# Kernel tuning notes

Measured on AMD Instinct MI355X. Metric: run time of the kernel, lower is better.

## Reference

```python
import jax, jax.numpy as jnp
import numpy as np

SEQ_LEN = 256
VOCAB = 50000
EMBED = 300
PROJ = 200
ATT = 200
CLS = 3
B = 128


def setup_inputs() -> dict:
    key = jax.random.key(0)
    ks = jax.random.split(key, 16)
    s = lambda d: 1.0 / np.sqrt(d)
    return {
        "x1": jax.random.randint(ks[0], (B, SEQ_LEN), 0, VOCAB, dtype=jnp.int32),
        "x2": jax.random.randint(ks[1], (B, SEQ_LEN), 0, VOCAB, dtype=jnp.int32),
        "emb": jax.random.normal(ks[2], (VOCAB, EMBED), jnp.float32),
        # intra-attention forward_product FC (shared for x1/x2 via AUTO_REUSE)
        "Wi": jax.random.normal(ks[3], (EMBED, ATT), jnp.float32) * s(EMBED),
        "bi": jnp.zeros((ATT,), jnp.float32),
        "b_dist": jax.random.normal(ks[4], (1,), jnp.float32) * 0.1,
        # embed-scope projection (input is concat[x, xp] -> 2*EMBED), linear
        "Wp": jax.random.normal(ks[5], (2 * EMBED, PROJ), jnp.float32) * s(2 * EMBED),
        "bp": jnp.zeros((PROJ,), jnp.float32),
        # attent forward_product FC (shared)
        "Wa": jax.random.normal(ks[6], (PROJ, ATT), jnp.float32) * s(PROJ),
        "ba": jnp.zeros((ATT,), jnp.float32),
        # compare FC (shared, dim = input dim = 2*PROJ)
        "Wc": jax.random.normal(ks[7], (2 * PROJ, 2 * PROJ), jnp.float32) * s(2 * PROJ),
        "bc": jnp.zeros((2 * PROJ,), jnp.float32),
        # aggregate FC -> class logits (linear)
        "Wg": jax.random.normal(ks[8], (4 * PROJ, CLS), jnp.float32) * s(4 * PROJ),
        "bg": jnp.zeros((CLS,), jnp.float32),
    }


def _seq_mask(x):
    # tf.count_nonzero + tf.sequence_mask -> [B, L, 1] float mask
    size = jnp.sum((x != 0).astype(jnp.float32), axis=1)  # [B]
    m = (jnp.arange(SEQ_LEN)[None, :] < size[:, None]).astype(jnp.float32)
    return m[:, :, None]


def _intra(x, Wi, bi, b_dist):
    # forward_product on (x, x): relu FC then bilinear product -> [B, L, L]
    f = jax.nn.relu(x @ Wi + bi)
    att = jnp.einsum("bid,bjd->bij", f, f)
    idx = jnp.arange(SEQ_LEN)
    dist = jnp.abs(idx[None, :] - idx[:, None])
    bias = b_dist[0] * (dist >= 10).astype(jnp.float32)  # [L, L]
    xp = jnp.einsum("bik,bkj->bij", jax.nn.softmax(att + bias[None], axis=2), x)
    return jnp.concatenate([x, xp], axis=2)  # [B, L, 2*EMBED]


def reference(x1, x2, emb, Wi, bi, b_dist, Wp, bp, Wa, ba, Wc, bc, Wg, bg):
    mask1, mask2 = _seq_mask(x1), _seq_mask(x2)  # [B, L, 1]

    # embedding lookup with L2-normalized table
    emb_n = emb / jnp.linalg.norm(emb, axis=1, keepdims=True)
    e1, e2 = emb_n[x1], emb_n[x2]  # [B, L, EMBED]

    # intra-attention (distance-biased self alignment), doubles feature dim
    h1 = _intra(e1, Wi, bi, b_dist)
    h2 = _intra(e2, Wi, bi, b_dist)

    # linear projection to PROJ
    p1 = h1 @ Wp + bp  # [B, L, PROJ]
    p2 = h2 @ Wp + bp

    # attent: forward_product sim + mask + dual-axis softmax alignments
    a1 = jax.nn.relu(p1 @ Wa + ba)
    a2 = jax.nn.relu(p2 @ Wa + ba)
    sim = jnp.einsum("bid,bjd->bij", a1, a2)  # [B, L, L]
    sim = sim * (mask1 * jnp.swapaxes(mask2, 1, 2))
    alpha = jnp.einsum("bki,bkj->bij", jax.nn.softmax(sim, axis=1), p1)
    beta = jnp.einsum("bik,bkj->bij", jax.nn.softmax(sim, axis=2), p2)

    # compare (shared relu FC)
    v1 = jax.nn.relu(jnp.concatenate([p1, beta], 2) @ Wc + bc)
    v2 = jax.nn.relu(jnp.concatenate([p2, alpha], 2) @ Wc + bc)

    # aggregate: masked sum pooling + linear classifier
    v1 = jnp.sum(v1 * mask1, axis=1)  # [B, 2*PROJ]
    v2 = jnp.sum(v2 * mask2, axis=1)
    return jnp.concatenate([v1, v2], 1) @ Wg + bg  # [B, CLS]
```

## Files before the change

### kernel.cpp

```cpp
#include <hip/hip_runtime.h>
#include <math.h>

#define LSEQ 256
#define NB   128

typedef unsigned short u16;
typedef unsigned int   u32;
typedef __attribute__((ext_vector_type(8))) short bf16x8;
typedef __attribute__((ext_vector_type(4))) float f32x4;

static __device__ __forceinline__ u16 f2bf(float x) {
    union { float f; u32 u; } v; v.f = x;
    const u32 r = v.u + 0x7fffu + ((v.u >> 16) & 1u);
    return (u16)(r >> 16);
}
static __device__ __forceinline__ u32 cvt_pk(float lo, float hi) {
    u32 r; asm("v_cvt_pk_bf16_f32 %0, %1, %2" : "=v"(r) : "v"(lo), "v"(hi));
    return r;
}
static __device__ __forceinline__ u16 f2bf_fast(float x) {
    u32 r; asm("v_cvt_pk_bf16_f32 %0, %1, %1" : "=v"(r) : "v"(x));
    return (u16)r;
}
static __device__ __forceinline__ void glds16(const u16* src, u16* dst) {
    __builtin_amdgcn_global_load_lds(
        (const __attribute__((address_space(1))) u32*)src,
        (__attribute__((address_space(3))) u32*)dst, 16, 0, 0);
}
static __device__ __forceinline__ void bar_lgkm() {
    asm volatile("s_waitcnt lgkmcnt(0)" ::: "memory");
    __builtin_amdgcn_s_barrier();
}
static __device__ __forceinline__ void bar_vm0() {
    asm volatile("s_waitcnt vmcnt(0)" ::: "memory");
    __builtin_amdgcn_s_barrier();
}

template<int EPI, bool BIAS, bool RELU>
__global__ __launch_bounds__(512)
void gemm(const u16* __restrict__ A, int lda,
          const u16* __restrict__ B, int ldb,
          u16* __restrict__ C, int ldc,
          const float* __restrict__ bias, int Nbias,
          float* __restrict__ pool, const float* __restrict__ pmask,
          int K, int Nwrite)
{
    __shared__ u16 As[128 * 64];
    __shared__ u16 Bs[256 * 64];

    const int m0 = blockIdx.y * 128;
    const int n0 = blockIdx.x * 256;
    const int t = threadIdx.x;
    const int lane = t & 63;
    const int w = t >> 6;
    const int wm = w >> 2;
    const int wn = w & 3;
    const int lr = lane & 15;
    const int lg = lane >> 4;

    f32x4 acc[4][4] = {};

    for (int k0 = 0; k0 < K; k0 += 64) {
#pragma unroll
        for (int i = 0; i < 2; ++i) {
            const int ch = w * 2 + i;
            const int row = (ch << 3) + (lane >> 3);
            const int slot = (lane & 7) ^ (row & 7);
            glds16(A + (long long)(m0 + row) * lda + k0 + (slot << 3), &As[ch << 9]);
        }
#pragma unroll
        for (int i = 0; i < 4; ++i) {
            const int ch = w * 4 + i;
            const int row = (ch << 3) + (lane >> 3);
            const int slot = (lane & 7) ^ (row & 7);
            glds16(B + (long long)(n0 + row) * ldb + k0 + (slot << 3), &Bs[ch << 9]);
        }
        __syncthreads();
#pragma unroll
        for (int kk = 0; kk < 2; ++kk) {
            bf16x8 af[4], bf[4];
#pragma unroll
            for (int mi = 0; mi < 4; ++mi) {
                const int row = wm * 64 + mi * 16 + lr;
                const int slot = ((kk << 2) + lg) ^ (row & 7);
                af[mi] = *reinterpret_cast<const bf16x8*>(&As[row * 64 + (slot << 3)]);
            }
#pragma unroll
            for (int ni = 0; ni < 4; ++ni) {
                const int row = wn * 64 + ni * 16 + lr;
                const int slot = ((kk << 2) + lg) ^ (row & 7);
                bf[ni] = *reinterpret_cast<const bf16x8*>(&Bs[row * 64 + (slot << 3)]);
            }
#pragma unroll
            for (int mi = 0; mi < 4; ++mi)
#pragma unroll
                for (int ni = 0; ni < 4; ++ni)
                    acc[mi][ni] = __builtin_amdgcn_mfma_f32_16x16x32_bf16(
                        af[mi], bf[ni], acc[mi][ni], 0, 0, 0);
        }
        __syncthreads();
    }

    const int rbase = lg << 2;
    if (EPI == 0) {
#pragma unroll
        for (int ni = 0; ni < 4; ++ni) {
            const int gc = n0 + wn * 64 + ni * 16 + lr;
            if (gc >= Nwrite) continue;
            float bcv = 0.f;
            if (BIAS) bcv = (gc < Nbias) ? bias[gc] : 0.f;
#pragma unroll
            for (int mi = 0; mi < 4; ++mi) {
#pragma unroll
                for (int r = 0; r < 4; ++r) {
                    const long long gr = m0 + wm * 64 + mi * 16 + rbase + r;
                    float x = acc[mi][ni][r];
                    if (BIAS) x += bcv;
                    if (RELU) x = fmaxf(x, 0.f);
                    C[gr * ldc + gc] = f2bf_fast(x);
                }
            }
        }
    } else {
        __syncthreads();
        float* pool_s = reinterpret_cast<float*>(As);
        for (int i = t; i < 256; i += 512) pool_s[i] = 0.f;
        __syncthreads();
        const int b_lin = m0 >> 8;
        const int side  = b_lin >> 7;
        const int bb    = b_lin & 127;
        const float* mk = pmask + b_lin * 256 + (m0 & 255);
        float mrow[4][4];
#pragma unroll
        for (int mi = 0; mi < 4; ++mi)
#pragma unroll
            for (int r = 0; r < 4; ++r)
                mrow[mi][r] = mk[wm * 64 + mi * 16 + rbase + r];
#pragma unroll
        for (int ni = 0; ni < 4; ++ni) {
            const int lc = wn * 64 + ni * 16 + lr;
            const int gc = n0 + lc;
            const float bcv = (BIAS && gc < Nbias) ? bias[gc] : 0.f;
            float cs = 0.f;
#pragma unroll
            for (int mi = 0; mi < 4; ++mi)
#pragma unroll
                for (int r = 0; r < 4; ++r)
                    cs += fmaxf(acc[mi][ni][r] + bcv, 0.f) * mrow[mi][r];
            cs += __shfl_xor(cs, 16, 64);
            cs += __shfl_xor(cs, 32, 64);
            if (lg == 0) atomicAdd(&pool_s[lc], cs);
        }
        __syncthreads();
        for (int i = t; i < 256; i += 512) {
            const int gc = n0 + i;
            if (gc < Nwrite) atomicAdd(&pool[bb * 800 + side * 400 + gc], pool_s[i]);
        }
    }
}

template<int MODE>
__global__ __launch_bounds__(512)
void fattn(const u16* __restrict__ QK, u16* __restrict__ Hb,
           u16* __restrict__ CMP, u16* __restrict__ CMP2,
           const float* __restrict__ M1, const float* __restrict__ M2,
           const float* __restrict__ b_dist)
{
    constexpr int NVT = (MODE == 0) ? 5 : 4;
    __shared__ __align__(16) char shmem[MODE == 0 ? 57344 : 49152];
    u16* Ks0 = (u16*)shmem;
    u16* Ks1 = (u16*)(shmem + 16384);
    u16* Qs0 = (u16*)(shmem + 32768);
    u16* Qs1 = (u16*)(shmem + 40960);
    u16* Pc = (u16*)shmem;
    u16* Vc = (u16*)(shmem + 16384);
    float* red  = (float*)shmem;
    float* red2 = red + 512;

    const int bz = blockIdx.x;
    int b, half, rowoff, ldv, ldc, Nwrite;
    const u16 *Kp, *Qp, *Vp;
    u16* Cp;
    const float *mrow = nullptr, *mcol = nullptr;
    if (MODE == 0) {
        b = (bz & 7) + (bz >> 4) * 8;
        half = (bz >> 3) & 1;
        Kp = QK + (long long)b * 65536;
        Qp = Kp;
        Vp = Hb + (long long)b * 163840; ldv = 640;
        Cp = Hb + (long long)b * 163840 + half * 128 * 640 + 320;
        ldc = 640; Nwrite = 320; rowoff = half * 128;
    } else {
        const int xcd = bz & 7, j = bz >> 3;
        const int sib = j & 3;
        b = xcd + (j >> 2) * 8;
        half = sib & 1;
        const int v = sib >> 1;
        const u16* a1 = QK + (long long)b * 65536;
        const u16* a2 = QK + 32768LL * 256 + (long long)b * 65536;
        u16* P1 = CMP  + (long long)b * 114688;
        u16* P2 = CMP2 + (long long)b * 114688;
        if (v == 0) { Qp = a1 + half * 128 * 256; Kp = a2; Vp = P2;
                      Cp = P1 + half * 128 * 448 + 200;
                      mrow = M1 + b * 256 + half * 128; mcol = M2 + b * 256; }
        else        { Qp = a2 + half * 128 * 256; Kp = a1; Vp = P1;
                      Cp = P2 + half * 128 * 448 + 200;
                      mrow = M2 + b * 256 + half * 128; mcol = M1 + b * 256; }
        ldv = 448; ldc = 448; Nwrite = 248; rowoff = 0;
    }

    const int t = threadIdx.x, lane = t & 63, w = t >> 6;
    const int lr = lane & 15, lg = lane >> 4;
    const int wk = w >> 1, wr = w & 1;
    const int wr2 = w >> 2, wc = w & 3;

    f32x4 acc[4][4] = {};
    {
        const int krow = (lane >> 2);
        const int kslot = (lane & 3) ^ (krow & 3);
#pragma unroll
        for (int i = 0; i < 2; ++i) {
            const int ch = w * 2 + i;
            glds16(Kp + (long long)(ch * 16 + krow) * 256 + (kslot << 3), Ks0 + (ch << 9));
        }
        if (MODE != 0)
            glds16(Qp + (long long)(w * 16 + krow) * 256 + (kslot << 3), Qs0 + (w << 9));
        for (int it = 0; it < 8; ++it) {
            bar_vm0();
            if (it < 7) {
                const int k0 = (it + 1) * 32;
                u16* kb2 = ((it + 1) & 1) ? Ks1 : Ks0;
#pragma unroll
                for (int i = 0; i < 2; ++i) {
                    const int ch = w * 2 + i;
                    glds16(Kp + (long long)(ch * 16 + krow) * 256 + k0 + (kslot << 3),
                           kb2 + (ch << 9));
                }
                if (MODE != 0) {
                    u16* qb2 = ((it + 1) & 1) ? Qs1 : Qs0;
                    glds16(Qp + (long long)(w * 16 + krow) * 256 + k0 + (kslot << 3),
                           qb2 + (w << 9));
                }
            }
            const u16* kb = (it & 1) ? Ks1 : Ks0;
            const u16* qb = (MODE == 0) ? kb : ((it & 1) ? Qs1 : Qs0);
            bf16x8 kf[4], qf[4];
#pragma unroll
            for (int ki = 0; ki < 4; ++ki) {
                const int row = wk * 64 + ki * 16 + lr;
                kf[ki] = *reinterpret_cast<const bf16x8*>(
                    &kb[row * 32 + ((lg ^ (row & 3)) << 3)]);
            }
#pragma unroll
            for (int qi = 0; qi < 4; ++qi) {
                const int row = (MODE == 0 ? rowoff : 0) + wr * 64 + qi * 16 + lr;
                qf[qi] = *reinterpret_cast<const bf16x8*>(
                    &qb[row * 32 + ((lg ^ (row & 3)) << 3)]);
            }
            __builtin_amdgcn_s_setprio(1);
#pragma unroll
            for (int ki = 0; ki < 4; ++ki)
#pragma unroll
                for (int qi = 0; qi < 4; ++qi)
                    acc[ki][qi] = __builtin_amdgcn_mfma_f32_16x16x32_bf16(
                        kf[ki], qf[qi], acc[ki][qi], 0, 0, 0);
            __builtin_amdgcn_s_setprio(0);
        }
    }

    if (MODE == 1) {
        float mr[4], mc[4][4];
#pragma unroll
        for (int qi = 0; qi < 4; ++qi) mr[qi] = mrow[wr * 64 + qi * 16 + lr];
#pragma unroll
        for (int ki = 0; ki < 4; ++ki)
#pragma unroll
            for (int r = 0; r < 4; ++r)
                mc[ki][r] = mcol[wk * 64 + ki * 16 + (lg << 2) + r];
#pragma unroll
        for (int ki = 0; ki < 4; ++ki)
#pragma unroll
            for (int qi = 0; qi < 4; ++qi)
#pragma unroll
                for (int r = 0; r < 4; ++r)
                    acc[ki][qi][r] *= mr[qi] * mc[ki][r];
    } else {
        const float bd = b_dist[0];
#pragma unroll
        for (int ki = 0; ki < 4; ++ki) {
            const int kb_ = wk * 64 + ki * 16;
#pragma unroll
            for (int qi = 0; qi < 4; ++qi) {
                const int qb_ = rowoff + wr * 64 + qi * 16;
                const int diff = qb_ - kb_;
                if (diff >= -24 && diff <= 24) {
                    const int irow = qb_ + lr;
                    const int jc0  = kb_ + (lg << 2);
#pragma unroll
                    for (int r = 0; r < 4; ++r) {
                        const int d = irow - (jc0 + r);
                        const int ad = d < 0 ? -d : d;
                        if (ad < 10) acc[ki][qi][r] -= bd;
                    }
                }
            }
        }
    }

    const int n4  = (t & 63) << 2;
    const int k8v = (t >> 6) << 3;
    const int n4b = 256 + ((t & 15) << 2);
    const int k8b = (t >> 4) << 3;
    uint2 vreg[8], vtail[8];
#pragma unroll
    for (int i = 0; i < 8; ++i)
        vreg[i] = *reinterpret_cast<const uint2*>(Vp + (long long)(k8v + i) * ldv + n4);
    if (NVT == 5) {
        if (t < 128) {
#pragma unroll
            for (int i = 0; i < 8; ++i)
                vtail[i] = *reinterpret_cast<const uint2*>(Vp + (long long)(k8b + i) * ldv + n4b);
        }
    }

    float mx[4];
#pragma unroll
    for (int qi = 0; qi < 4; ++qi) {
        float m_ = -1e30f;
#pragma unroll
        for (int ki = 0; ki < 4; ++ki)
#pragma unroll
            for (int r = 0; r < 4; ++r) m_ = fmaxf(m_, acc[ki][qi][r]);
        m_ = fmaxf(m_, __shfl_xor(m_, 16, 64));
        m_ = fmaxf(m_, __shfl_xor(m_, 32, 64));
        mx[qi] = m_;
    }
    if (lg == 0) {
#pragma unroll
        for (int qi = 0; qi < 4; ++qi)
            red[(wr * 64 + qi * 16 + lr) * 4 + wk] = mx[qi];
    }
    bar_lgkm();
    float sm[4];
#pragma unroll
    for (int qi = 0; qi < 4; ++qi) {
        const int row = wr * 64 + qi * 16 + lr;
        const float m_ = fmaxf(fmaxf(red[row * 4 + 0], red[row * 4 + 1]),
                               fmaxf(red[row * 4 + 2], red[row * 4 + 3]));
        float s_ = 0.f;
#pragma unroll
        for (int ki = 0; ki < 4; ++ki)
#pragma unroll
            for (int r = 0; r < 4; ++r) {
                const float e_ = __expf(acc[ki][qi][r] - m_);
                acc[ki][qi][r] = e_;
                s_ += e_;
            }
        s_ += __shfl_xor(s_, 16, 64);
        s_ += __shfl_xor(s_, 32, 64);
        sm[qi] = s_;
    }
    if (lg == 0) {
#pragma unroll
        for (int qi = 0; qi < 4; ++qi)
            red2[(wr * 64 + qi * 16 + lr) * 4 + wk] = sm[qi];
    }
    bar_lgkm();
#pragma unroll
    for (int qi = 0; qi < 4; ++qi) {
        const int row = wr * 64 + qi * 16 + lr;
        const float rs = 1.0f / (red2[row * 4 + 0] + red2[row * 4 + 1]
                               + red2[row * 4 + 2] + red2[row * 4 + 3]);
#pragma unroll
        for (int ki = 0; ki < 4; ++ki)
#pragma unroll
            for (int r = 0; r < 4; ++r) acc[ki][qi][r] *= rs;
    }
    bar_lgkm();

    f32x4 opv[4][NVT] = {};
    for (int c = 0; c < 4; ++c) {
        {
            union { uint2 q2[8]; u16 s[32]; } uq;
#pragma unroll
            for (int i = 0; i < 8; ++i) uq.q2[i] = vreg[i];
#pragma unroll
            for (int j = 0; j < 4; ++j) {
                const int row = n4 + j;
                const u32 v0 = (u32)uq.s[j]      | ((u32)uq.s[4 + j]  << 16);
                const u32 v1 = (u32)uq.s[8 + j]  | ((u32)uq.s[12 + j] << 16);
                const u32 v2 = (u32)uq.s[16 + j] | ((u32)uq.s[20 + j] << 16);
                const u32 v3 = (u32)uq.s[24 + j] | ((u32)uq.s[28 + j] << 16);
                const int slot = (t >> 6) ^ (row & 7);
                *reinterpret_cast<uint4*>(&Vc[row * 64 + (slot << 3)]) =
                    make_uint4(v0, v1, v2, v3);
            }
            if (NVT == 5 && t < 128) {
                union { uint2 q2[8]; u16 s[32]; } ub;
#pragma unroll
                for (int i = 0; i < 8; ++i) ub.q2[i] = vtail[i];
#pragma unroll
                for (int j = 0; j < 4; ++j) {
                    const int row = n4b + j;
                    const u32 v0 = (u32)ub.s[j]      | ((u32)ub.s[4 + j]  << 16);
                    const u32 v1 = (u32)ub.s[8 + j]  | ((u32)ub.s[12 + j] << 16);
                    const u32 v2 = (u32)ub.s[16 + j] | ((u32)ub.s[20 + j] << 16);
                    const u32 v3 = (u32)ub.s[24 + j] | ((u32)ub.s[28 + j] << 16);
                    const int slot = (t >> 4) ^ (row & 7);
                    *reinterpret_cast<uint4*>(&Vc[row * 64 + (slot << 3)]) =
                        make_uint4(v0, v1, v2, v3);
                }
            }
        }
        if (wk == c) {
#pragma unroll
            for (int qi = 0; qi < 4; ++qi) {
                const int qrow = wr * 64 + qi * 16 + lr;
#pragma unroll
                for (int ki = 0; ki < 4; ++ki) {
                    const u32 lo = cvt_pk(acc[ki][qi][0], acc[ki][qi][1]);
                    const u32 hi = cvt_pk(acc[ki][qi][2], acc[ki][qi][3]);
                    const int slot = ((ki << 1) + (lg >> 1)) ^ (qrow & 7);
                    *reinterpret_cast<uint2*>(
                        (char*)Pc + qrow * 128 + (slot << 4) + ((lg & 1) << 3)) =
                        make_uint2(lo, hi);
                }
            }
        }
        if (c < 3) {
#pragma unroll
            for (int i = 0; i < 8; ++i)
                vreg[i] = *reinterpret_cast<const uint2*>(
                    Vp + (long long)((c + 1) * 64 + k8v + i) * ldv + n4);
            if (NVT == 5 && t < 128) {
#pragma unroll
                for (int i = 0; i < 8; ++i)
                    vtail[i] = *reinterpret_cast<const uint2*>(
                        Vp + (long long)((c + 1) * 64 + k8b + i) * ldv + n4b);
            }
        }
        bar_lgkm();
#pragma unroll
        for (int kk = 0; kk < 2; ++kk) {
            bf16x8 pa[4], vb[NVT];
#pragma unroll
            for (int qi = 0; qi < 4; ++qi) {
                const int row = wr2 * 64 + qi * 16 + lr;
                const int slot = ((kk << 2) + lg) ^ (row & 7);
                pa[qi] = *reinterpret_cast<const bf16x8*>(&Pc[row * 64 + (slot << 3)]);
            }
#pragma unroll
            for (int vi = 0; vi < NVT; ++vi) {
                const int row = wc * (NVT * 16) + vi * 16 + lr;
                const int slot = ((kk << 2) + lg) ^ (row & 7);
                vb[vi] = *reinterpret_cast<const bf16x8*>(&Vc[row * 64 + (slot << 3)]);
            }
            __builtin_amdgcn_s_setprio(1);
#pragma unroll
            for (int qi = 0; qi < 4; ++qi)
#pragma unroll
                for (int vi = 0; vi < NVT; ++vi)
                    opv[qi][vi] = __builtin_amdgcn_mfma_f32_16x16x32_bf16(
                        pa[qi], vb[vi], opv[qi][vi], 0, 0, 0);
            __builtin_amdgcn_s_setprio(0);
        }
        bar_lgkm();
    }

#pragma unroll
    for (int qi = 0; qi < 4; ++qi)
#pragma unroll
        for (int vi = 0; vi < NVT; ++vi) {
            const int gc = wc * (NVT * 16) + vi * 16 + lr;
            if (gc >= Nwrite) continue;
#pragma unroll
            for (int r = 0; r < 4; ++r) {
                const int qrow = wr2 * 64 + qi * 16 + (lg << 2) + r;
                Cp[(long long)qrow * ldc + gc] = f2bf_fast(opv[qi][vi][r]);
            }
        }
}

__global__ __launch_bounds__(256)
void prep_all(const int* __restrict__ x1, const int* __restrict__ x2,
              const float* __restrict__ emb,
              const float* __restrict__ Wi, const float* __restrict__ Wa,
              const float* __restrict__ Wp, const float* __restrict__ Wc,
              u16* __restrict__ h,
              u16* __restrict__ WiT, u16* __restrict__ WaT,
              u16* __restrict__ WpT, u16* __restrict__ WcT,
              float* __restrict__ M1f, float* __restrict__ POOL)
{
    const int blk = blockIdx.x;
    const int t = threadIdx.x;
    if (blk < 16384) {
        const int lane = t & 63;
        const long long row = (long long)blk * 4 + (t >> 6);
        const int tok = (row < 32768) ? x1[row] : x2[row - 32768];
        const float* er = emb + (long long)tok * 300;
        float vals[5];
        float ss = 0.f;
#pragma unroll
        for (int i = 0; i < 5; ++i) {
            const int c = lane + i * 64;
            const float v = (c < 300) ? er[c] : 0.f;
            vals[i] = v;
            ss = fmaf(v, v, ss);
        }
#pragma unroll
        for (int o = 32; o; o >>= 1) ss += __shfl_xor(ss, o, 64);
        const float inv = 1.0f / sqrtf(ss);
        u16* outp = h + row * 640;
#pragma unroll
        for (int i = 0; i < 5; ++i) {
            const int c = lane + i * 64;
            outp[c] = f2bf(vals[i] * inv);
        }
    } else if (blk < 18496) {
        int idx = (blk - 16384) * 256 + t;
        const float* src; u16* dst; int srcRows, srcCols, dstCols, seg1, seg2;
        if (idx < 81920)       { src = Wi; dst = WiT; srcRows = 300; srcCols = 200; dstCols = 320; seg1 = 300; seg2 = 320; }
        else if (idx < 147456) { idx -= 81920;  src = Wa; dst = WaT; srcRows = 200; srcCols = 200; dstCols = 256; seg1 = 200; seg2 = 256; }
        else if (idx < 311296) { idx -= 147456; src = Wp; dst = WpT; srcRows = 600; srcCols = 200; dstCols = 640; seg1 = 300; seg2 = 320; }
        else                   { idx -= 311296; src = Wc; dst = WcT; srcRows = 400; srcCols = 400; dstCols = 448; seg1 = 400; seg2 = 448; }
        const int n = idx / dstCols, k = idx - n * dstCols;
        int sr = -1;
        if (k < seg1) sr = k;
        else if (k >= seg2 && (k - seg2) < (srcRows - seg1)) sr = seg1 + (k - seg2);
        u16 v = 0;
        if (n < srcCols && sr >= 0) v = f2bf(src[(long long)sr * srcCols + n]);
        dst[idx] = v;
    } else {
        const int b2 = blk - 18496;
        const int b = b2 & 127;
        const int* x = (b2 < 128) ? x1 : x2;
        float* mask = M1f + (b2 < 128 ? 0 : 32768);
        int nz = (x[b * LSEQ + t] != 0) ? 1 : 0;
#pragma unroll
        for (int o = 32; o; o >>= 1) nz += __shfl_xor(nz, o, 64);
        __shared__ int red[4];
        if ((t & 63) == 0) red[t >> 6] = nz;
        __syncthreads();
        const int size = red[0] + red[1] + red[2] + red[3];
        mask[b * LSEQ + t] = (t < size) ? 1.0f : 0.0f;
        if (b2 < 128) {
            for (int i = t; i < 800; i += 256) POOL[b * 800 + i] = 0.f;
        }
    }
}

__global__ __launch_bounds__(256)
void final_fc(const float* __restrict__ pooled, const float* __restrict__ Wg,
              const float* __restrict__ bg, float* __restrict__ out)
{
    const int b = blockIdx.x;
    const int t = threadIdx.x;
    float a0 = 0.f, a1 = 0.f, a2 = 0.f;
    for (int k = t; k < 800; k += 256) {
        const float p = pooled[(long long)b * 800 + k];
        a0 = fmaf(p, Wg[k * 3 + 0], a0);
        a1 = fmaf(p, Wg[k * 3 + 1], a1);
        a2 = fmaf(p, Wg[k * 3 + 2], a2);
    }
#pragma unroll
    for (int o = 32; o; o >>= 1) {
        a0 += __shfl_xor(a0, o, 64);
        a1 += __shfl_xor(a1, o, 64);
        a2 += __shfl_xor(a2, o, 64);
    }
    __shared__ float r0[4], r1[4], r2[4];
    if ((t & 63) == 0) { r0[t >> 6] = a0; r1[t >> 6] = a1; r2[t >> 6] = a2; }
    __syncthreads();
    if (t == 0) {
        out[b * 3 + 0] = r0[0] + r0[1] + r0[2] + r0[3] + bg[0];
        out[b * 3 + 1] = r1[0] + r1[1] + r1[2] + r1[3] + bg[1];
        out[b * 3 + 2] = r2[0] + r2[1] + r2[2] + r2[3] + bg[2];
    }
}

extern "C" void kernel_launch(void* const* d_in, const int* in_sizes, int n_in,
                              void* d_out, int out_size, void* d_ws, size_t ws_size,
                              hipStream_t stream)
{
    (void)in_sizes; (void)n_in; (void)out_size; (void)ws_size;

    const int*   x1     = (const int*)  d_in[0];
    const int*   x2     = (const int*)  d_in[1];
    const float* emb    = (const float*)d_in[2];
    const float* Wi     = (const float*)d_in[3];
    const float* bi     = (const float*)d_in[4];
    const float* b_dist = (const float*)d_in[5];
    const float* Wp     = (const float*)d_in[6];
    const float* bp     = (const float*)d_in[7];
    const float* Wa     = (const float*)d_in[8];
    const float* ba     = (const float*)d_in[9];
    const float* Wc     = (const float*)d_in[10];
    const float* bc     = (const float*)d_in[11];
    const float* Wg     = (const float*)d_in[12];
    const float* bg     = (const float*)d_in[13];
    float* out = (float*)d_out;

    u16* wsu  = (u16*)d_ws;
    u16* H    = wsu;
    u16* CMP  = wsu + 41943040;
    u16* FA   = wsu + 71303168;
    u16* WiT  = wsu + 88080384;
    u16* WaT  = wsu + 88162304;
    u16* WpT  = wsu + 88227840;
    u16* WcT  = wsu + 88391680;
    float* fb = (float*)(wsu + 88621056);
    float* POOL = fb;
    float* M1f  = fb + 102400;
    float* M2f  = fb + 135168;

    u16* CMP2 = CMP + (long long)32768 * 448;

    prep_all<<<18752, 256, 0, stream>>>(x1, x2, emb, Wi, Wa, Wp, Wc,
                                        H, WiT, WaT, WpT, WcT, M1f, POOL);

    gemm<0, true, true><<<dim3(1, 512, 1), 512, 0, stream>>>(
        H, 640, WiT, 320, FA, 256, bi, 200, nullptr, nullptr, 320, 256);
    fattn<0><<<512, 512, 0, stream>>>(FA, H, nullptr, nullptr, nullptr, nullptr, b_dist);
    gemm<0, true, false><<<dim3(1, 512, 1), 512, 0, stream>>>(
        H, 640, WpT, 640, CMP, 448, bp, 200, nullptr, nullptr, 640, 256);
    gemm<0, true, true><<<dim3(1, 512, 1), 512, 0, stream>>>(
        CMP, 448, WaT, 256, FA, 256, ba, 200, nullptr, nullptr, 256, 256);
    fattn<1><<<512, 512, 0, stream>>>(FA, nullptr, CMP, CMP2, M1f, M2f, nullptr);
    gemm<2, true, true><<<dim3(2, 512, 1), 512, 0, stream>>>(
        CMP, 448, WcT, 448, nullptr, 0, bc, 400, POOL, M1f, 448, 400);

    final_fc<<<NB, 256, 0, stream>>>(POOL, Wg, bg, out);
}
```

Measured before the change: 198.5 us.

## Triple-buffer K tiles with partial vmcnt waits and a new LDS swizzle

```diff
diff --git a/kernel.cpp b/kernel.cpp
--- a/kernel.cpp
+++ b/kernel.cpp
@@ -29,10 +29,6 @@
 }
 static __device__ __forceinline__ void bar_lgkm() {
     asm volatile("s_waitcnt lgkmcnt(0)" ::: "memory");
-    __builtin_amdgcn_s_barrier();
-}
-static __device__ __forceinline__ void bar_vm0() {
-    asm volatile("s_waitcnt vmcnt(0)" ::: "memory");
     __builtin_amdgcn_s_barrier();
 }
 
@@ -167,11 +163,7 @@
            const float* __restrict__ b_dist)
 {
     constexpr int NVT = (MODE == 0) ? 5 : 4;
-    __shared__ __align__(16) char shmem[MODE == 0 ? 57344 : 49152];
-    u16* Ks0 = (u16*)shmem;
-    u16* Ks1 = (u16*)(shmem + 16384);
-    u16* Qs0 = (u16*)(shmem + 32768);
-    u16* Qs1 = (u16*)(shmem + 40960);
+    __shared__ __align__(16) char shmem[MODE == 0 ? 57344 : 65536];
     u16* Pc = (u16*)shmem;
     u16* Vc = (u16*)(shmem + 16384);
     float* red  = (float*)shmem;
@@ -216,46 +208,57 @@
 
     f32x4 acc[4][4] = {};
     {
-        const int krow = (lane >> 2);
-        const int kslot = (lane & 3) ^ (krow & 3);
+        const int krow = lane >> 2;
+        const int kslot = (lane & 3) ^ ((krow ^ (krow >> 2)) & 3);
+        if (MODE != 0)
+            glds16(Qp + (long long)(w * 16 + krow) * 256 + (kslot << 3),
+                   (u16*)(shmem + 49152) + (w << 9));
 #pragma unroll
         for (int i = 0; i < 2; ++i) {
             const int ch = w * 2 + i;
-            glds16(Kp + (long long)(ch * 16 + krow) * 256 + (kslot << 3), Ks0 + (ch << 9));
-        }
-        if (MODE != 0)
-            glds16(Qp + (long long)(w * 16 + krow) * 256 + (kslot << 3), Qs0 + (w << 9));
+            glds16(Kp + (long long)(ch * 16 + krow) * 256 + (kslot << 3),
+                   (u16*)shmem + (ch << 9));
+        }
+#pragma unroll
+        for (int i = 0; i < 2; ++i) {
+            const int ch = w * 2 + i;
+            glds16(Kp + (long long)(ch * 16 + krow) * 256 + 32 + (kslot << 3),
+                   (u16*)(shmem + 16384) + (ch << 9));
+        }
+#pragma unroll
         for (int it = 0; it < 8; ++it) {
-            bar_vm0();
-            if (it < 7) {
-                const int k0 = (it + 1) * 32;
-                u16* kb2 = ((it + 1) & 1) ? Ks1 : Ks0;
+            if (it == 7) asm volatile("s_waitcnt vmcnt(0)" ::: "memory");
+            else         asm volatile("s_waitcnt vmcnt(2)" ::: "memory");
+            __builtin_amdgcn_s_barrier();
+            if (MODE != 0 && it < 7) {
+                u16* qb2 = (u16*)(shmem + 49152 + (((it + 1) & 1) << 13));
+                glds16(Qp + (long long)(w * 16 + krow) * 256 + (it + 1) * 32 + (kslot << 3),
+                       qb2 + (w << 9));
+            }
+            if (it < 6) {
+                u16* kb2 = (u16*)(shmem + ((it + 2) % 3) * 16384);
 #pragma unroll
                 for (int i = 0; i < 2; ++i) {
                     const int ch = w * 2 + i;
-                    glds16(Kp + (long long)(ch * 16 + krow) * 256 + k0 + (kslot << 3),
+                    glds16(Kp + (long long)(ch * 16 + krow) * 256 + (it + 2) * 32 + (kslot << 3),
                            kb2 + (ch << 9));
                 }
-                if (MODE != 0) {
-                    u16* qb2 = ((it + 1) & 1) ? Qs1 : Qs0;
-                    glds16(Qp + (long long)(w * 16 + krow) * 256 + k0 + (kslot << 3),
-                           qb2 + (w << 9));
-                }
-            }
-            const u16* kb = (it & 1) ? Ks1 : Ks0;
-            const u16* qb = (MODE == 0) ? kb : ((it & 1) ? Qs1 : Qs0);
+            }
+            const u16* kb = (const u16*)(shmem + (it % 3) * 16384);
+            const u16* qb = (MODE == 0) ? kb
+                          : (const u16*)(shmem + 49152 + ((it & 1) << 13));
             bf16x8 kf[4], qf[4];
 #pragma unroll
             for (int ki = 0; ki < 4; ++ki) {
                 const int row = wk * 64 + ki * 16 + lr;
-                kf[ki] = *reinterpret_cast<const bf16x8*>(
-                    &kb[row * 32 + ((lg ^ (row & 3)) << 3)]);
+                const int phys = lg ^ ((row ^ (row >> 2)) & 3);
+                kf[ki] = *reinterpret_cast<const bf16x8*>(&kb[row * 32 + (phys << 3)]);
             }
 #pragma unroll
             for (int qi = 0; qi < 4; ++qi) {
                 const int row = (MODE == 0 ? rowoff : 0) + wr * 64 + qi * 16 + lr;
-                qf[qi] = *reinterpret_cast<const bf16x8*>(
-                    &qb[row * 32 + ((lg ^ (row & 3)) << 3)]);
+                const int phys = lg ^ ((row ^ (row >> 2)) & 3);
+                qf[qi] = *reinterpret_cast<const bf16x8*>(&qb[row * 32 + (phys << 3)]);
             }
             __builtin_amdgcn_s_setprio(1);
 #pragma unroll
```

Result: no change. 196.7 us (-0.9%).
